# Performance work log

Measured on AMD Instinct MI355X. Metric: run time of the kernel, lower is better.

Reference implementation:

```python
import jax, jax.numpy as jnp
import numpy as np

N_USER = 100000
N_ITEM = 50000
N = N_USER + N_ITEM
N_EDGES = 1200000
D = 64
NEG_SLOPE = 0.01  # torch leaky_relu default
EPS = 1e-12       # torch F.normalize default


def setup_inputs() -> dict:
    key = jax.random.key(0)
    ks = jax.random.split(key, 9)
    user_emb = jax.random.normal(ks[0], (N_USER, D), dtype=jnp.float32) * 0.1
    item_emb = jax.random.normal(ks[1], (N_ITEM, D), dtype=jnp.float32) * 0.1
    edge_row = jax.random.randint(ks[2], (N_EDGES,), 0, N, dtype=jnp.int32)
    edge_col = jax.random.randint(ks[3], (N_EDGES,), 0, N, dtype=jnp.int32)
    edge_val = jax.random.uniform(ks[4], (N_EDGES,), dtype=jnp.float32)
    Wf = jax.random.normal(ks[5], (3, D, D), dtype=jnp.float32) * (1.0 / np.sqrt(D))
    bf = jnp.zeros((3, D), dtype=jnp.float32)
    Wb = jax.random.normal(ks[6], (3, D, D), dtype=jnp.float32) * (1.0 / np.sqrt(D))
    bb = jnp.zeros((3, D), dtype=jnp.float32)
    return {"user_emb": user_emb, "item_emb": item_emb,
            "edge_row": edge_row, "edge_col": edge_col, "edge_val": edge_val,
            "Wf": Wf, "bf": bf, "Wb": Wb, "bb": bb}


def _spmm_plus_eye(edge_row, edge_col, edge_val, E):
    # (H + I) @ E : gather source features, scale, segment-sum into rows, add E
    msgs = edge_val[:, None] * E[edge_col]          # [n_edges, D]
    agg = jax.ops.segment_sum(msgs, edge_row, num_segments=N)
    return agg + E


def reference(user_emb, item_emb, edge_row, edge_col, edge_val, Wf, bf, Wb, bb):
    E_l = jnp.concatenate([user_emb, item_emb], axis=0)  # [N, D]
    all_emb = [E_l]
    for i in range(3):
        front = _spmm_plus_eye(edge_row, edge_col, edge_val, E_l)
        front_cal = jax.nn.leaky_relu(front @ Wf[i].T + bf[i], NEG_SLOPE)
        back = jax.nn.leaky_relu((E_l * front) @ Wb[i].T + bb[i], NEG_SLOPE)
        E_l = front_cal + back  # dropout p=0.5 treated as eval-mode identity
        norm = jnp.maximum(jnp.linalg.norm(E_l, axis=1, keepdims=True), EPS)
        all_emb.append(E_l / norm)
    all_emb = jnp.concatenate(all_emb, axis=1)  # [N, 4*D]
    return all_emb[:N_USER], all_emb[N_USER:]
```

## Files before the change

kernel.cpp:

```cpp
#include <hip/hip_runtime.h>
#include <hip/hip_bf16.h>
#include <stdint.h>

#define N_USER 100000
#define N_ITEM 50000
#define NTOT   150000
#define NEDGE  1200000
#define D      64
#define OUTD   256
#define NEG    0.01f
#define NBLK   586
#define LSTR   65
#define INITBLK 9375

typedef __attribute__((ext_vector_type(8))) short short8;
typedef __attribute__((ext_vector_type(4))) float f32x4;

__device__ inline ushort f2bf(float x) {
    uint32_t u = __float_as_uint(x);
    u += 0x7fffu + ((u >> 16) & 1u);
    return (ushort)(u >> 16);
}
__device__ inline void split2(float x, ushort& h, ushort& l) {
    ushort hh = f2bf(x);
    float hf = __uint_as_float(((uint32_t)hh) << 16);
    h = hh;
    l = f2bf(x - hf);
}
__device__ inline void split8(const float* p, short8& h8, short8& l8) {
    float4 v0 = *(const float4*)p;
    float4 v1 = *(const float4*)(p + 4);
    float vv[8] = {v0.x, v0.y, v0.z, v0.w, v1.x, v1.y, v1.z, v1.w};
    #pragma unroll
    for (int e = 0; e < 8; e++) {
        ushort h, l;
        split2(vv[e], h, l);
        h8[e] = (short)h; l8[e] = (short)l;
    }
}

__global__ void k_init_hist(const float* __restrict__ ue, const float* __restrict__ ie,
                            float* __restrict__ E, float* __restrict__ out,
                            const int* __restrict__ row, int* __restrict__ cnt) {
    if (blockIdx.x < INITBLK) {
        int t = blockIdx.x * 256 + threadIdx.x;
        int r = t >> 4, q = t & 15;
        const float* src = (r < N_USER) ? (ue + (size_t)r * D)
                                        : (ie + (size_t)(r - N_USER) * D);
        float4 v = *(const float4*)(src + q * 4);
        *(float4*)(E + (size_t)r * D + q * 4) = v;
        *(float4*)(out + (size_t)r * OUTD + q * 4) = v;
    } else {
        int e = (blockIdx.x - INITBLK) * 256 + threadIdx.x;
        if (e < NEDGE) atomicAdd(&cnt[row[e]], 1);
    }
}

__global__ void k_scan_a(const int* __restrict__ cnt, int* __restrict__ part) {
    __shared__ int s[4];
    int i = blockIdx.x * 256 + threadIdx.x;
    int v = (i < NTOT) ? cnt[i] : 0;
    for (int off = 32; off; off >>= 1) v += __shfl_down(v, off, 64);
    if ((threadIdx.x & 63) == 0) s[threadIdx.x >> 6] = v;
    __syncthreads();
    if (threadIdx.x == 0) part[blockIdx.x] = s[0] + s[1] + s[2] + s[3];
}

__global__ void k_scan_b(int* __restrict__ part) {
    __shared__ int s[1024];
    int t = threadIdx.x;
    int v = (t < NBLK) ? part[t] : 0;
    s[t] = v;
    __syncthreads();
    for (int off = 1; off < 1024; off <<= 1) {
        int x = (t >= off) ? s[t - off] : 0;
        __syncthreads();
        s[t] += x;
        __syncthreads();
    }
    if (t < NBLK) part[t] = s[t] - v;
}

__global__ void k_scan_c(const int* __restrict__ cnt, const int* __restrict__ part,
                         int* __restrict__ offs, int* __restrict__ cur) {
    __shared__ int ws[4];
    int i = blockIdx.x * 256 + threadIdx.x;
    int v = (i < NTOT) ? cnt[i] : 0;
    int lane = threadIdx.x & 63, w = threadIdx.x >> 6;
    int x = v;
    for (int o = 1; o < 64; o <<= 1) {
        int y = __shfl_up(x, o, 64);
        if (lane >= o) x += y;
    }
    if (lane == 63) ws[w] = x;
    __syncthreads();
    int base = part[blockIdx.x];
    for (int k = 0; k < w; k++) base += ws[k];
    int excl = base + x - v;
    if (i < NTOT) { offs[i] = excl; cur[i] = excl; }
    if (i == 0) offs[NTOT] = NEDGE;
}

__global__ void k_scatter(const int* __restrict__ row, const int* __restrict__ col,
                          const float* __restrict__ val, int* __restrict__ cur,
                          int2* __restrict__ ce) {
    int e = blockIdx.x * blockDim.x + threadIdx.x;
    if (e >= NEDGE) return;
    int r = row[e];
    int p = atomicAdd(&cur[r], 1);
    int2 u;
    u.x = col[e];
    u.y = __float_as_int(val[e]);
    ce[p] = u;
}

__global__ __launch_bounds__(256) void k_layer(
    const float* __restrict__ Ecur, float* __restrict__ Enx,
    const int* __restrict__ offs, const int2* __restrict__ ce,
    const float* __restrict__ Wf, const float* __restrict__ bfv,
    const float* __restrict__ Wb, const float* __restrict__ bbv,
    float* __restrict__ out, int chunk) {
    __shared__ float sf[16 * LSTR];
    __shared__ float sg[16 * LSTR];
    __shared__ float nrm[16][4];

    int t    = threadIdx.x;
    int lane = t & 63;
    int w    = t >> 6;
    int cl   = lane & 15;
    int kg   = lane >> 4;
    int r0   = blockIdx.x * 16;

    int col = w * 16 + cl;
    short8 wfh0, wfl0, wbh0, wbl0, wfh1, wfl1, wbh1, wbl1;
    split8(Wf + (size_t)col * D +  0 + kg * 8, wfh0, wfl0);
    split8(Wb + (size_t)col * D +  0 + kg * 8, wbh0, wbl0);
    split8(Wf + (size_t)col * D + 32 + kg * 8, wfh1, wfl1);
    split8(Wb + (size_t)col * D + 32 + kg * 8, wbh1, wbl1);
    float bF = bfv[col], bB = bbv[col];

    {
        int row = w * 4 + kg;
        int d4  = cl * 4;
        int r   = r0 + row;
        float4 ei = *(const float4*)(Ecur + (size_t)r * D + d4);
        float4 a0 = ei;
        float4 a1 = {0.f,0.f,0.f,0.f}, a2 = {0.f,0.f,0.f,0.f}, a3 = {0.f,0.f,0.f,0.f};
        int s = offs[r], e = offs[r + 1];
        int p = s;
        for (; p + 4 <= e; p += 4) {
            int2 c0 = ce[p + 0];
            int2 c1 = ce[p + 1];
            int2 c2 = ce[p + 2];
            int2 c3 = ce[p + 3];
            float4 x0 = *(const float4*)(Ecur + (size_t)c0.x * D + d4);
            float4 x1 = *(const float4*)(Ecur + (size_t)c1.x * D + d4);
            float4 x2 = *(const float4*)(Ecur + (size_t)c2.x * D + d4);
            float4 x3 = *(const float4*)(Ecur + (size_t)c3.x * D + d4);
            float v0 = __int_as_float(c0.y), v1 = __int_as_float(c1.y);
            float v2 = __int_as_float(c2.y), v3 = __int_as_float(c3.y);
            a0.x = fmaf(v0, x0.x, a0.x); a0.y = fmaf(v0, x0.y, a0.y);
            a0.z = fmaf(v0, x0.z, a0.z); a0.w = fmaf(v0, x0.w, a0.w);
            a1.x = fmaf(v1, x1.x, a1.x); a1.y = fmaf(v1, x1.y, a1.y);
            a1.z = fmaf(v1, x1.z, a1.z); a1.w = fmaf(v1, x1.w, a1.w);
            a2.x = fmaf(v2, x2.x, a2.x); a2.y = fmaf(v2, x2.y, a2.y);
            a2.z = fmaf(v2, x2.z, a2.z); a2.w = fmaf(v2, x2.w, a2.w);
            a3.x = fmaf(v3, x3.x, a3.x); a3.y = fmaf(v3, x3.y, a3.y);
            a3.z = fmaf(v3, x3.z, a3.z); a3.w = fmaf(v3, x3.w, a3.w);
        }
        for (; p < e; ++p) {
            int2 c = ce[p];
            float v = __int_as_float(c.y);
            float4 x = *(const float4*)(Ecur + (size_t)c.x * D + d4);
            a0.x = fmaf(v, x.x, a0.x); a0.y = fmaf(v, x.y, a0.y);
            a0.z = fmaf(v, x.z, a0.z); a0.w = fmaf(v, x.w, a0.w);
        }
        float4 fr;
        fr.x = (a0.x + a1.x) + (a2.x + a3.x);
        fr.y = (a0.y + a1.y) + (a2.y + a3.y);
        fr.z = (a0.z + a1.z) + (a2.z + a3.z);
        fr.w = (a0.w + a1.w) + (a2.w + a3.w);
        float4 gv;
        gv.x = fr.x * ei.x; gv.y = fr.y * ei.y;
        gv.z = fr.z * ei.z; gv.w = fr.w * ei.w;
        *(float4*)(sf + row * LSTR + d4) = fr;
        *(float4*)(sg + row * LSTR + d4) = gv;
    }
    __syncthreads();

    f32x4 accF = {0.f, 0.f, 0.f, 0.f};
    f32x4 accB = {0.f, 0.f, 0.f, 0.f};
    {
        short8 fh, fl, gh, gl;
        split8(sf + cl * LSTR +  0 + kg * 8, fh, fl);
        split8(sg + cl * LSTR +  0 + kg * 8, gh, gl);
        accF = __builtin_amdgcn_mfma_f32_16x16x32_bf16(fh, wfh0, accF, 0, 0, 0);
        accB = __builtin_amdgcn_mfma_f32_16x16x32_bf16(gh, wbh0, accB, 0, 0, 0);
        accF = __builtin_amdgcn_mfma_f32_16x16x32_bf16(fl, wfh0, accF, 0, 0, 0);
        accB = __builtin_amdgcn_mfma_f32_16x16x32_bf16(gl, wbh0, accB, 0, 0, 0);
        accF = __builtin_amdgcn_mfma_f32_16x16x32_bf16(fh, wfl0, accF, 0, 0, 0);
        accB = __builtin_amdgcn_mfma_f32_16x16x32_bf16(gh, wbl0, accB, 0, 0, 0);
        split8(sf + cl * LSTR + 32 + kg * 8, fh, fl);
        split8(sg + cl * LSTR + 32 + kg * 8, gh, gl);
        accF = __builtin_amdgcn_mfma_f32_16x16x32_bf16(fh, wfh1, accF, 0, 0, 0);
        accB = __builtin_amdgcn_mfma_f32_16x16x32_bf16(gh, wbh1, accB, 0, 0, 0);
        accF = __builtin_amdgcn_mfma_f32_16x16x32_bf16(fl, wfh1, accF, 0, 0, 0);
        accB = __builtin_amdgcn_mfma_f32_16x16x32_bf16(gl, wbh1, accB, 0, 0, 0);
        accF = __builtin_amdgcn_mfma_f32_16x16x32_bf16(fh, wfl1, accF, 0, 0, 0);
        accB = __builtin_amdgcn_mfma_f32_16x16x32_bf16(gh, wbl1, accB, 0, 0, 0);
    }

    float e4[4], p4[4];
    #pragma unroll
    for (int rg = 0; rg < 4; rg++) {
        float aF = accF[rg] + bF;
        float aB = accB[rg] + bB;
        float vF = (aF > 0.f) ? aF : NEG * aF;
        float vB = (aB > 0.f) ? aB : NEG * aB;
        float e = vF + vB;
        e4[rg] = e;
        float p = e * e;
        p += __shfl_xor(p, 1, 64);
        p += __shfl_xor(p, 2, 64);
        p += __shfl_xor(p, 4, 64);
        p += __shfl_xor(p, 8, 64);
        p4[rg] = p;
    }
    if (cl == 0) {
        #pragma unroll
        for (int rg = 0; rg < 4; rg++) nrm[kg * 4 + rg][w] = p4[rg];
    }
    __syncthreads();
    #pragma unroll
    for (int rg = 0; rg < 4; rg++) {
        int row = kg * 4 + rg;
        float4 nv = *(const float4*)&nrm[row][0];
        float nsq = (nv.x + nv.y) + (nv.z + nv.w);
        float inv = 1.0f / fmaxf(sqrtf(nsq), 1e-12f);
        Enx[(size_t)(r0 + row) * D + col] = e4[rg];
        out[(size_t)(r0 + row) * OUTD + (size_t)chunk * D + col] = e4[rg] * inv;
    }
}

extern "C" void kernel_launch(void* const* d_in, const int* in_sizes, int n_in,
                              void* d_out, int out_size, void* d_ws, size_t ws_size,
                              hipStream_t stream) {
    const float* ue   = (const float*)d_in[0];
    const float* ie   = (const float*)d_in[1];
    const int*   erow = (const int*)d_in[2];
    const int*   ecol = (const int*)d_in[3];
    const float* eval = (const float*)d_in[4];
    const float* Wf   = (const float*)d_in[5];
    const float* bfv  = (const float*)d_in[6];
    const float* Wb   = (const float*)d_in[7];
    const float* bbv  = (const float*)d_in[8];
    float* out = (float*)d_out;

    float* E0   = (float*)d_ws;
    float* E1   = E0 + (size_t)NTOT * D;
    int*   cnt  = (int*)(E1 + (size_t)NTOT * D);
    int*   offs = cnt + NTOT;
    int*   cur  = offs + NTOT + 1;
    int*   part = cur + NTOT;
    int2*  ce   = (int2*)(part + 1024);

    hipMemsetAsync(cnt, 0, NTOT * sizeof(int), stream);
    k_init_hist<<<INITBLK + (NEDGE + 255) / 256, 256, 0, stream>>>(ue, ie, E0, out, erow, cnt);
    k_scan_a<<<NBLK, 256, 0, stream>>>(cnt, part);
    k_scan_b<<<1, 1024, 0, stream>>>(part);
    k_scan_c<<<NBLK, 256, 0, stream>>>(cnt, part, offs, cur);
    k_scatter<<<(NEDGE + 255) / 256, 256, 0, stream>>>(erow, ecol, eval, cur, ce);

    const float* rd[3] = {E0, E1, E0};
    float*       wr[3] = {E1, E0, E1};
    for (int i = 0; i < 3; i++) {
        k_layer<<<NTOT / 16, 256, 0, stream>>>(
            rd[i], wr[i], offs, ce,
            Wf + (size_t)i * D * D, bfv + (size_t)i * D,
            Wb + (size_t)i * D * D, bbv + (size_t)i * D, out, i + 1);
    }
}
```

Baseline: 730.4 us.

## Balance SpMM across block edges with LDS atomics and pre-split weights

The per-row gather loop is replaced by a block-level loop over all edges of the block's 16 rows, with each edge tagged with its local row in the high bits of the column index. Contributions are accumulated into shared memory with float atomics, which evens out work when row degrees vary. Weights are split into bf16 hi/lo once in the init kernel and then loaded directly, and activations are split once into LDS instead of per MFMA lane. This adds LDS atomic contention and makes the floating-point summation order nondeterministic.

```diff
diff --git a/kernel.cpp b/kernel.cpp
--- a/kernel.cpp
+++ b/kernel.cpp
@@ -11,7 +11,10 @@
 #define NEG    0.01f
 #define NBLK   586
 #define LSTR   65
+#define SSTR   72
 #define INITBLK 9375
+#define HISTBLK 4688
+#define WPREPBLK 24
 
 typedef __attribute__((ext_vector_type(8))) short short8;
 typedef __attribute__((ext_vector_type(4))) float f32x4;
@@ -41,7 +44,9 @@
 
 __global__ void k_init_hist(const float* __restrict__ ue, const float* __restrict__ ie,
                             float* __restrict__ E, float* __restrict__ out,
-                            const int* __restrict__ row, int* __restrict__ cnt) {
+                            const int* __restrict__ row, int* __restrict__ cnt,
+                            const float* __restrict__ Wf, const float* __restrict__ Wb,
+                            ushort* __restrict__ wpre) {
     if (blockIdx.x < INITBLK) {
         int t = blockIdx.x * 256 + threadIdx.x;
         int r = t >> 4, q = t & 15;
@@ -50,9 +55,24 @@
         float4 v = *(const float4*)(src + q * 4);
         *(float4*)(E + (size_t)r * D + q * 4) = v;
         *(float4*)(out + (size_t)r * OUTD + q * 4) = v;
-    } else {
+    } else if (blockIdx.x < INITBLK + HISTBLK) {
         int e = (blockIdx.x - INITBLK) * 256 + threadIdx.x;
         if (e < NEDGE) atomicAdd(&cnt[row[e]], 1);
+    } else {
+        int u = (blockIdx.x - INITBLK - HISTBLK) * 256 + threadIdx.x;
+        if (u < 6144) {
+            int p  = u & 1;
+            int kg = (u >> 1) & 3;
+            int s  = (u >> 3) & 1;
+            int c  = (u >> 4) & 63;
+            int m  = (u >> 10) & 1;
+            int L  = u >> 11;
+            const float* W = m ? Wb : Wf;
+            const float* src = W + (size_t)L * 4096 + c * 64 + s * 32 + kg * 8;
+            short8 h8, l8;
+            split8(src, h8, l8);
+            *(short8*)(wpre + (size_t)u * 8) = p ? l8 : h8;
+        }
     }
 }
 
@@ -109,7 +129,7 @@
     int r = row[e];
     int p = atomicAdd(&cur[r], 1);
     int2 u;
-    u.x = col[e];
+    u.x = col[e] | ((r & 15) << 18);
     u.y = __float_as_int(val[e]);
     ce[p] = u;
 }
@@ -117,91 +137,113 @@
 __global__ __launch_bounds__(256) void k_layer(
     const float* __restrict__ Ecur, float* __restrict__ Enx,
     const int* __restrict__ offs, const int2* __restrict__ ce,
-    const float* __restrict__ Wf, const float* __restrict__ bfv,
-    const float* __restrict__ Wb, const float* __restrict__ bbv,
-    float* __restrict__ out, int chunk) {
-    __shared__ float sf[16 * LSTR];
-    __shared__ float sg[16 * LSTR];
-    __shared__ float nrm[16][4];
+    const ushort* __restrict__ wpre, const float* __restrict__ bfv,
+    const float* __restrict__ bbv, float* __restrict__ out, int chunk) {
+    __shared__ __align__(16) float  sf [16 * LSTR];
+    __shared__ __align__(16) ushort sfh[16 * SSTR], sfl[16 * SSTR];
+    __shared__ __align__(16) ushort sgh[16 * SSTR], sgl[16 * SSTR];
+    __shared__ __align__(16) float  nrm[16][4];
 
     int t    = threadIdx.x;
-    int lane = t & 63;
-    int w    = t >> 6;
-    int cl   = lane & 15;
-    int kg   = lane >> 4;
     int r0   = blockIdx.x * 16;
-
-    int col = w * 16 + cl;
-    short8 wfh0, wfl0, wbh0, wbl0, wfh1, wfl1, wbh1, wbl1;
-    split8(Wf + (size_t)col * D +  0 + kg * 8, wfh0, wfl0);
-    split8(Wb + (size_t)col * D +  0 + kg * 8, wbh0, wbl0);
-    split8(Wf + (size_t)col * D + 32 + kg * 8, wfh1, wfl1);
-    split8(Wb + (size_t)col * D + 32 + kg * 8, wbh1, wbl1);
+    int row  = t >> 4;
+    int lid  = t & 15;
+    int d4   = lid * 4;
+
+    float4 ei = *(const float4*)(Ecur + (size_t)(r0 + row) * D + d4);
+    *(float4*)(sf + row * LSTR + d4) = ei;
+
+    int lane = t & 63, w = t >> 6;
+    int cl   = lane & 15, kg = lane >> 4;
+    int col  = w * 16 + cl;
+
+    short8 wfh0, wfl0, wfh1, wfl1, wbh0, wbl0, wbh1, wbl1;
+    {
+        const ushort* bp = wpre;
+        #define WLD(m, s, p) (*(const short8*)(bp + (size_t)((((((m)*64+col)*2+(s))*4+kg)*2+(p))*8)))
+        wfh0 = WLD(0, 0, 0); wfl0 = WLD(0, 0, 1);
+        wfh1 = WLD(0, 1, 0); wfl1 = WLD(0, 1, 1);
+        wbh0 = WLD(1, 0, 0); wbl0 = WLD(1, 0, 1);
+        wbh1 = WLD(1, 1, 0); wbl1 = WLD(1, 1, 1);
+        #undef WLD
+    }
     float bF = bfv[col], bB = bbv[col];
 
+    __syncthreads();
+
     {
-        int row = w * 4 + kg;
-        int d4  = cl * 4;
-        int r   = r0 + row;
-        float4 ei = *(const float4*)(Ecur + (size_t)r * D + d4);
-        float4 a0 = ei;
-        float4 a1 = {0.f,0.f,0.f,0.f}, a2 = {0.f,0.f,0.f,0.f}, a3 = {0.f,0.f,0.f,0.f};
-        int s = offs[r], e = offs[r + 1];
-        int p = s;
-        for (; p + 4 <= e; p += 4) {
-            int2 c0 = ce[p + 0];
-            int2 c1 = ce[p + 1];
-            int2 c2 = ce[p + 2];
-            int2 c3 = ce[p + 3];
-            float4 x0 = *(const float4*)(Ecur + (size_t)c0.x * D + d4);
-            float4 x1 = *(const float4*)(Ecur + (size_t)c1.x * D + d4);
-            float4 x2 = *(const float4*)(Ecur + (size_t)c2.x * D + d4);
-            float4 x3 = *(const float4*)(Ecur + (size_t)c3.x * D + d4);
+        int base = offs[r0];
+        int n    = offs[r0 + 16] - base;
+        int i = row;
+        for (; i + 48 < n; i += 64) {
+            int2 c0 = ce[base + i];
+            int2 c1 = ce[base + i + 16];
+            int2 c2 = ce[base + i + 32];
+            int2 c3 = ce[base + i + 48];
+            float4 x0 = *(const float4*)(Ecur + (size_t)(c0.x & 0x3FFFF) * D + d4);
+            float4 x1 = *(const float4*)(Ecur + (size_t)(c1.x & 0x3FFFF) * D + d4);
+            float4 x2 = *(const float4*)(Ecur + (size_t)(c2.x & 0x3FFFF) * D + d4);
+            float4 x3 = *(const float4*)(Ecur + (size_t)(c3.x & 0x3FFFF) * D + d4);
             float v0 = __int_as_float(c0.y), v1 = __int_as_float(c1.y);
             float v2 = __int_as_float(c2.y), v3 = __int_as_float(c3.y);
-            a0.x = fmaf(v0, x0.x, a0.x); a0.y = fmaf(v0, x0.y, a0.y);
-            a0.z = fmaf(v0, x0.z, a0.z); a0.w = fmaf(v0, x0.w, a0.w);
-            a1.x = fmaf(v1, x1.x, a1.x); a1.y = fmaf(v1, x1.y, a1.y);
-            a1.z = fmaf(v1, x1.z, a1.z); a1.w = fmaf(v1, x1.w, a1.w);
-            a2.x = fmaf(v2, x2.x, a2.x); a2.y = fmaf(v2, x2.y, a2.y);
-            a2.z = fmaf(v2, x2.z, a2.z); a2.w = fmaf(v2, x2.w, a2.w);
-            a3.x = fmaf(v3, x3.x, a3.x); a3.y = fmaf(v3, x3.y, a3.y);
-            a3.z = fmaf(v3, x3.z, a3.z); a3.w = fmaf(v3, x3.w, a3.w);
+            float* p0 = sf + (c0.x >> 18) * LSTR + d4;
+            float* p1 = sf + (c1.x >> 18) * LSTR + d4;
+            float* p2 = sf + (c2.x >> 18) * LSTR + d4;
+            float* p3 = sf + (c3.x >> 18) * LSTR + d4;
+            atomicAdd(p0 + 0, v0 * x0.x); atomicAdd(p0 + 1, v0 * x0.y);
+            atomicAdd(p0 + 2, v0 * x0.z); atomicAdd(p0 + 3, v0 * x0.w);
+            atomicAdd(p1 + 0, v1 * x1.x); atomicAdd(p1 + 1, v1 * x1.y);
+            atomicAdd(p1 + 2, v1 * x1.z); atomicAdd(p1 + 3, v1 * x1.w);
+            atomicAdd(p2 + 0, v2 * x2.x); atomicAdd(p2 + 1, v2 * x2.y);
+            atomicAdd(p2 + 2, v2 * x2.z); atomicAdd(p2 + 3, v2 * x2.w);
+            atomicAdd(p3 + 0, v3 * x3.x); atomicAdd(p3 + 1, v3 * x3.y);
+            atomicAdd(p3 + 2, v3 * x3.z); atomicAdd(p3 + 3, v3 * x3.w);
         }
-        for (; p < e; ++p) {
-            int2 c = ce[p];
+        for (; i < n; i += 16) {
+            int2 c = ce[base + i];
+            float4 x = *(const float4*)(Ecur + (size_t)(c.x & 0x3FFFF) * D + d4);
             float v = __int_as_float(c.y);
-            float4 x = *(const float4*)(Ecur + (size_t)c.x * D + d4);
-            a0.x = fmaf(v, x.x, a0.x); a0.y = fmaf(v, x.y, a0.y);
-            a0.z = fmaf(v, x.z, a0.z); a0.w = fmaf(v, x.w, a0.w);
+            float* p = sf + (c.x >> 18) * LSTR + d4;
+            atomicAdd(p + 0, v * x.x); atomicAdd(p + 1, v * x.y);
+            atomicAdd(p + 2, v * x.z); atomicAdd(p + 3, v * x.w);
         }
-        float4 fr;
-        fr.x = (a0.x + a1.x) + (a2.x + a3.x);
-        fr.y = (a0.y + a1.y) + (a2.y + a3.y);
-        fr.z = (a0.z + a1.z) + (a2.z + a3.z);
-        fr.w = (a0.w + a1.w) + (a2.w + a3.w);
+    }
+    __syncthreads();
+
+    {
+        float4 fr = *(const float4*)(sf + row * LSTR + d4);
         float4 gv;
         gv.x = fr.x * ei.x; gv.y = fr.y * ei.y;
         gv.z = fr.z * ei.z; gv.w = fr.w * ei.w;
-        *(float4*)(sf + row * LSTR + d4) = fr;
-        *(float4*)(sg + row * LSTR + d4) = gv;
+        ushort h0,l0,h1,l1,h2,l2,h3,l3;
+        split2(fr.x, h0, l0); split2(fr.y, h1, l1);
+        split2(fr.z, h2, l2); split2(fr.w, h3, l3);
+        *(ushort4*)(sfh + row * SSTR + d4) = make_ushort4(h0, h1, h2, h3);
+        *(ushort4*)(sfl + row * SSTR + d4) = make_ushort4(l0, l1, l2, l3);
+        split2(gv.x, h0, l0); split2(gv.y, h1, l1);
+        split2(gv.z, h2, l2); split2(gv.w, h3, l3);
+        *(ushort4*)(sgh + row * SSTR + d4) = make_ushort4(h0, h1, h2, h3);
+        *(ushort4*)(sgl + row * SSTR + d4) = make_ushort4(l0, l1, l2, l3);
     }
     __syncthreads();
 
     f32x4 accF = {0.f, 0.f, 0.f, 0.f};
     f32x4 accB = {0.f, 0.f, 0.f, 0.f};
     {
-        short8 fh, fl, gh, gl;
-        split8(sf + cl * LSTR +  0 + kg * 8, fh, fl);
-        split8(sg + cl * LSTR +  0 + kg * 8, gh, gl);
+        short8 fh = *(const short8*)(sfh + cl * SSTR +  0 + kg * 8);
+        short8 fl = *(const short8*)(sfl + cl * SSTR +  0 + kg * 8);
+        short8 gh = *(const short8*)(sgh + cl * SSTR +  0 + kg * 8);
+        short8 gl = *(const short8*)(sgl + cl * SSTR +  0 + kg * 8);
         accF = __builtin_amdgcn_mfma_f32_16x16x32_bf16(fh, wfh0, accF, 0, 0, 0);
         accB = __builtin_amdgcn_mfma_f32_16x16x32_bf16(gh, wbh0, accB, 0, 0, 0);
         accF = __builtin_amdgcn_mfma_f32_16x16x32_bf16(fl, wfh0, accF, 0, 0, 0);
         accB = __builtin_amdgcn_mfma_f32_16x16x32_bf16(gl, wbh0, accB, 0, 0, 0);
         accF = __builtin_amdgcn_mfma_f32_16x16x32_bf16(fh, wfl0, accF, 0, 0, 0);
         accB = __builtin_amdgcn_mfma_f32_16x16x32_bf16(gh, wbl0, accB, 0, 0, 0);
-        split8(sf + cl * LSTR + 32 + kg * 8, fh, fl);
-        split8(sg + cl * LSTR + 32 + kg * 8, gh, gl);
+        fh = *(const short8*)(sfh + cl * SSTR + 32 + kg * 8);
+        fl = *(const short8*)(sfl + cl * SSTR + 32 + kg * 8);
+        gh = *(const short8*)(sgh + cl * SSTR + 32 + kg * 8);
+        gl = *(const short8*)(sgl + cl * SSTR + 32 + kg * 8);
         accF = __builtin_amdgcn_mfma_f32_16x16x32_bf16(fh, wfh1, accF, 0, 0, 0);
         accB = __builtin_amdgcn_mfma_f32_16x16x32_bf16(gh, wbh1, accB, 0, 0, 0);
         accF = __builtin_amdgcn_mfma_f32_16x16x32_bf16(fl, wfh1, accF, 0, 0, 0);
@@ -233,12 +275,12 @@
     __syncthreads();
     #pragma unroll
     for (int rg = 0; rg < 4; rg++) {
-        int row = kg * 4 + rg;
-        float4 nv = *(const float4*)&nrm[row][0];
+        int rr = kg * 4 + rg;
+        float4 nv = *(const float4*)&nrm[rr][0];
         float nsq = (nv.x + nv.y) + (nv.z + nv.w);
         float inv = 1.0f / fmaxf(sqrtf(nsq), 1e-12f);
-        Enx[(size_t)(r0 + row) * D + col] = e4[rg];
-        out[(size_t)(r0 + row) * OUTD + (size_t)chunk * D + col] = e4[rg] * inv;
+        Enx[(size_t)(r0 + rr) * D + col] = e4[rg];
+        out[(size_t)(r0 + rr) * OUTD + (size_t)chunk * D + col] = e4[rg] * inv;
     }
 }
 
@@ -256,16 +298,18 @@
     const float* bbv  = (const float*)d_in[8];
     float* out = (float*)d_out;
 
-    float* E0   = (float*)d_ws;
-    float* E1   = E0 + (size_t)NTOT * D;
-    int*   cnt  = (int*)(E1 + (size_t)NTOT * D);
-    int*   offs = cnt + NTOT;
-    int*   cur  = offs + NTOT + 1;
-    int*   part = cur + NTOT;
-    int2*  ce   = (int2*)(part + 1024);
+    float*  E0   = (float*)d_ws;
+    float*  E1   = E0 + (size_t)NTOT * D;
+    ushort* wpre = (ushort*)(E1 + (size_t)NTOT * D);
+    int*    cnt  = (int*)(wpre + 49152);
+    int*    offs = cnt + NTOT;
+    int*    cur  = offs + NTOT + 2;
+    int*    part = cur + NTOT;
+    int2*   ce   = (int2*)(part + 1024);
 
     hipMemsetAsync(cnt, 0, NTOT * sizeof(int), stream);
-    k_init_hist<<<INITBLK + (NEDGE + 255) / 256, 256, 0, stream>>>(ue, ie, E0, out, erow, cnt);
+    k_init_hist<<<INITBLK + HISTBLK + WPREPBLK, 256, 0, stream>>>(
+        ue, ie, E0, out, erow, cnt, Wf, Wb, wpre);
     k_scan_a<<<NBLK, 256, 0, stream>>>(cnt, part);
     k_scan_b<<<1, 1024, 0, stream>>>(part);
     k_scan_c<<<NBLK, 256, 0, stream>>>(cnt, part, offs, cur);
@@ -276,7 +320,7 @@
     for (int i = 0; i < 3; i++) {
         k_layer<<<NTOT / 16, 256, 0, stream>>>(
             rd[i], wr[i], offs, ce,
-            Wf + (size_t)i * D * D, bfv + (size_t)i * D,
-            Wb + (size_t)i * D * D, bbv + (size_t)i * D, out, i + 1);
-    }
-}
+            wpre + (size_t)i * 16384, bfv + (size_t)i * D,
+            bbv + (size_t)i * D, out, i + 1);
+    }
+}
```

After: 1.571 ms. +115.2%, slower.
